# Kernel optimization log

Measured on AMD Instinct MI355X. Metric: run time of the kernel, lower is better.

The kernel has to match this reference:

```python
import jax, jax.numpy as jnp
import numpy as np

N, E, F_IN, EDIM, H = 50000, 1600000, 128, 16, 4
C1, C2, G, NCLS = 32, 8, 64, 10
NEG_SLOPE = 0.2


def setup_inputs() -> dict:
    key = jax.random.key(0)
    ks = jax.random.split(key, 20)
    s = 0.1
    inp = {
        "x": jax.random.normal(ks[0], (N, F_IN), jnp.float32),
        "edge_index": jax.random.randint(ks[1], (2, E), 0, N, dtype=jnp.int32),
        "edge_attr": jax.random.normal(ks[2], (E, EDIM), jnp.float32),
        "batch": jnp.sort(jax.random.randint(ks[3], (N,), 0, G, dtype=jnp.int32)),
        # layer 1 params (PyG GATConv: shared lin for src/dst, no lin bias)
        "W1": jax.random.normal(ks[4], (F_IN, H * C1), jnp.float32) * s,
        "as1": jax.random.normal(ks[5], (H, C1), jnp.float32) * s,
        "ad1": jax.random.normal(ks[6], (H, C1), jnp.float32) * s,
        "We1": jax.random.normal(ks[7], (EDIM, H * C1), jnp.float32) * s,
        "ae1": jax.random.normal(ks[8], (H, C1), jnp.float32) * s,
        "b1": jnp.zeros((H * C1,), jnp.float32),
        # layer 2 params
        "W2": jax.random.normal(ks[9], (H * C1, H * C2), jnp.float32) * s,
        "as2": jax.random.normal(ks[10], (H, C2), jnp.float32) * s,
        "ad2": jax.random.normal(ks[11], (H, C2), jnp.float32) * s,
        "We2": jax.random.normal(ks[12], (EDIM, H * C2), jnp.float32) * s,
        "ae2": jax.random.normal(ks[13], (H, C2), jnp.float32) * s,
        "b2": jnp.zeros((H * C2,), jnp.float32),
        # final linear
        "Wfc": jax.random.normal(ks[14], (H * C2, NCLS), jnp.float32) * s,
        "bfc": jnp.zeros((NCLS,), jnp.float32),
    }
    return inp


def _add_self_loops(src, dst, edge_attr):
    # PyG default: add_self_loops=True, fill_value='mean' (mean of incoming edge attrs)
    deg = jax.ops.segment_sum(jnp.ones((E,), jnp.float32), dst, num_segments=N)
    loop_attr = jax.ops.segment_sum(edge_attr, dst, num_segments=N) / jnp.maximum(deg, 1.0)[:, None]
    loop = jnp.arange(N, dtype=src.dtype)
    return (jnp.concatenate([src, loop]), jnp.concatenate([dst, loop]),
            jnp.concatenate([edge_attr, loop_attr], axis=0))


def _gat_layer(x, src, dst, ea, W, a_src, a_dst, We, a_e, b, heads, ch):
    n = x.shape[0]
    h = (x @ W).reshape(n, heads, ch)                 # [N,H,C]
    he = (ea @ We).reshape(-1, heads, ch)             # [Ef,H,C]
    al_src = jnp.einsum('nhc,hc->nh', h, a_src)       # [N,H]
    al_dst = jnp.einsum('nhc,hc->nh', h, a_dst)
    al_e = jnp.einsum('ehc,hc->eh', he, a_e)          # [Ef,H]
    alpha = al_src[src] + al_dst[dst] + al_e
    alpha = jax.nn.leaky_relu(alpha, NEG_SLOPE)
    # edge softmax grouped by destination node
    amax = jax.ops.segment_max(alpha, dst, num_segments=n)
    alpha = jnp.exp(alpha - amax[dst])
    denom = jax.ops.segment_sum(alpha, dst, num_segments=n)
    alpha = alpha / (denom[dst] + 1e-16)
    out = jax.ops.segment_sum(h[src] * alpha[..., None], dst, num_segments=n)  # [N,H,C]
    return out.reshape(n, heads * ch) + b


def reference(x, edge_index, edge_attr, batch, W1, as1, ad1, We1, ae1, b1,
              W2, as2, ad2, We2, ae2, b2, Wfc, bfc):
    src, dst = edge_index[0], edge_index[1]
    src, dst, ea = _add_self_loops(src, dst, edge_attr)
    h = jax.nn.relu(_gat_layer(x, src, dst, ea, W1, as1, ad1, We1, ae1, b1, H, C1))
    h = jax.nn.relu(_gat_layer(h, src, dst, ea, W2, as2, ad2, We2, ae2, b2, H, C2))
    # global mean pool over graphs
    cnt = jax.ops.segment_sum(jnp.ones((N,), jnp.float32), batch, num_segments=G)
    pooled = jax.ops.segment_sum(h, batch, num_segments=G) / jnp.maximum(cnt, 1.0)[:, None]
    return pooled @ Wfc + bfc
```

## Files before the change

### kernel.cpp

```cpp
#include <hip/hip_runtime.h>
#include <hip/hip_fp16.h>
#include <math.h>

typedef float4 f4;
#define NEG_SLOPE 0.2f
#define NBMAX 1024
#define BIN_CHUNK 8192

union h4pack { float2 f; __half2 h[2]; };

__global__ void k_prep(const float* __restrict__ We1, const float* __restrict__ ae1,
                       const float* __restrict__ We2, const float* __restrict__ ae2,
                       float* __restrict__ M) {
    int t = threadIdx.x;
    if (t >= 128) return;
    int sel = t >> 6, i = t & 63, d = i >> 2, h = i & 3;
    const float* W  = sel ? We2 : We1;
    const float* ae = sel ? ae2 : ae1;
    int C = sel ? 8 : 32, ncol = sel ? 32 : 128;
    float s = 0.f;
    for (int c = 0; c < C; ++c) s += W[d * ncol + h * C + c] * ae[h * C + c];
    M[sel * 64 + d * 4 + h] = s;
}

__global__ __launch_bounds__(256) void k_bhist(const int* __restrict__ ei,
                                               int* __restrict__ bcnt, int E, int NB) {
    __shared__ int hist[NBMAX];
    for (int i = threadIdx.x; i < NB; i += 256) hist[i] = 0;
    __syncthreads();
    int stride = gridDim.x * 256;
    for (int e = blockIdx.x * 256 + threadIdx.x; e < E; e += stride)
        atomicAdd(&hist[ei[E + e] >> 6], 1);
    __syncthreads();
    for (int i = threadIdx.x; i < NB; i += 256) {
        int h = hist[i];
        if (h) atomicAdd(&bcnt[i], h);
    }
}

__global__ void k_bscan(const int* __restrict__ bcnt, int* __restrict__ bprefix,
                        int* __restrict__ bcursor, int NB) {
    __shared__ int ts[NBMAX];
    int t = threadIdx.x;
    ts[t] = (t < NB) ? bcnt[t] : 0;
    __syncthreads();
    for (int off = 1; off < 1024; off <<= 1) {
        int v = (t >= off) ? ts[t - off] : 0;
        __syncthreads();
        ts[t] += v;
        __syncthreads();
    }
    int excl = (t == 0) ? 0 : ts[t - 1];
    if (t <= NB) {
        bprefix[t] = excl;
        if (t < NB) bcursor[t] = excl;
    }
}

__global__ void k_ale_lin(const float* __restrict__ ea, const float* __restrict__ Mbuf,
                          __half* __restrict__ ale1_e, __half* __restrict__ ale2_e, int E) {
    __shared__ float Ms[128];
    if (threadIdx.x < 128) Ms[threadIdx.x] = Mbuf[threadIdx.x];
    __syncthreads();
    int e = blockIdx.x * 256 + threadIdx.x;
    if (e >= E) return;
    const f4* row = (const f4*)(ea + (size_t)e * 16);
    f4 r0 = row[0], r1 = row[1], r2 = row[2], r3 = row[3];
    float a[16] = { r0.x, r0.y, r0.z, r0.w, r1.x, r1.y, r1.z, r1.w,
                    r2.x, r2.y, r2.z, r2.w, r3.x, r3.y, r3.z, r3.w };
    float s10 = 0.f, s11 = 0.f, s12 = 0.f, s13 = 0.f;
    float s20 = 0.f, s21 = 0.f, s22 = 0.f, s23 = 0.f;
#pragma unroll
    for (int dd = 0; dd < 16; ++dd) {
        float av = a[dd];
        s10 += av * Ms[dd * 4 + 0]; s11 += av * Ms[dd * 4 + 1];
        s12 += av * Ms[dd * 4 + 2]; s13 += av * Ms[dd * 4 + 3];
        s20 += av * Ms[64 + dd * 4 + 0]; s21 += av * Ms[64 + dd * 4 + 1];
        s22 += av * Ms[64 + dd * 4 + 2]; s23 += av * Ms[64 + dd * 4 + 3];
    }
    h4pack p1, p2;
    p1.h[0] = __floats2half2_rn(s10, s11); p1.h[1] = __floats2half2_rn(s12, s13);
    p2.h[0] = __floats2half2_rn(s20, s21); p2.h[1] = __floats2half2_rn(s22, s23);
    ((float2*)ale1_e)[e] = p1.f;
    ((float2*)ale2_e)[e] = p2.f;
}

__global__ __launch_bounds__(256) void k_bin(const int* __restrict__ ei,
                                             int* __restrict__ bcursor,
                                             int2* __restrict__ binned, int E, int NB) {
    __shared__ int hist[NBMAX], base[NBMAX], cur[NBMAX];
    for (int i = threadIdx.x; i < NB; i += 256) { hist[i] = 0; cur[i] = 0; }
    __syncthreads();
    int e0 = blockIdx.x * BIN_CHUNK;
    int e1 = min(e0 + BIN_CHUNK, E);
    for (int e = e0 + threadIdx.x; e < e1; e += 256)
        atomicAdd(&hist[ei[E + e] >> 6], 1);
    __syncthreads();
    for (int i = threadIdx.x; i < NB; i += 256) {
        int h = hist[i];
        if (h) base[i] = atomicAdd(&bcursor[i], h);
    }
    __syncthreads();
    for (int e = e0 + threadIdx.x; e < e1; e += 256) {
        int sr = ei[e], d = ei[E + e];
        int b = d >> 6;
        int loc = base[b] + atomicAdd(&cur[b], 1);
        binned[loc] = make_int2(sr, ((d & 63) << 26) | e);
    }
}

__global__ __launch_bounds__(256) void k_csr(const int2* __restrict__ binned,
                                             const int* __restrict__ bprefix,
                                             int* __restrict__ offsets,
                                             int2* __restrict__ csr_se,
                                             int N, int E, int NB) {
    __shared__ int nhist[64], noff[65];
    int b = blockIdx.x;
    if (threadIdx.x < 64) nhist[threadIdx.x] = 0;
    __syncthreads();
    int lo = bprefix[b], hi = bprefix[b + 1];
    for (int s = lo + threadIdx.x; s < hi; s += 256)
        atomicAdd(&nhist[(binned[s].y >> 26) & 63], 1);
    __syncthreads();
    if (threadIdx.x == 0) {
        int run = 0;
        for (int i = 0; i < 64; ++i) { noff[i] = run; run += nhist[i]; }
        noff[64] = run;
    }
    __syncthreads();
    int nlo = b << 6;
    int nbn = min(64, N - nlo);
    if (threadIdx.x < nbn) offsets[nlo + threadIdx.x] = lo + noff[threadIdx.x];
    if (b == NB - 1 && threadIdx.x == 0) offsets[N] = E;
    if (threadIdx.x < 64) nhist[threadIdx.x] = 0;
    __syncthreads();
    for (int s = lo + threadIdx.x; s < hi; s += 256) {
        int2 r = binned[s];
        int dl = (r.y >> 26) & 63;
        int slot = lo + noff[dl] + atomicAdd(&nhist[dl], 1);
        csr_se[slot] = make_int2(r.x, r.y & 0x03FFFFFF);
    }
}

template<int NOUT, int ROWS>
__global__ __launch_bounds__(256) void k_gemm(const float* __restrict__ X,
                                              const float* __restrict__ W,
                                              __half* __restrict__ Hout, int N) {
    __shared__ __align__(16) float xs[ROWS][128];
    int row0 = blockIdx.x * ROWS;
    int tid = threadIdx.x;
    constexpr int NF4 = ROWS * 32;
    const f4* x4 = (const f4*)X;
    for (int i = tid; i < NF4; i += 256) {
        int r = i >> 5, k4 = i & 31;
        f4 v;
        if (row0 + r < N) v = x4[(size_t)(row0 + r) * 32 + k4];
        else { v.x = v.y = v.z = v.w = 0.f; }
        ((f4*)&xs[r][0])[k4] = v;
    }
    __syncthreads();
    constexpr int GRP = 256 / NOUT;
    constexpr int PR  = ROWS / GRP;
    int col = tid % NOUT, rg = tid / NOUT;
    float acc[PR];
#pragma unroll
    for (int r = 0; r < PR; ++r) acc[r] = 0.f;
    for (int k = 0; k < 128; ++k) {
        float w = W[k * NOUT + col];
#pragma unroll
        for (int r = 0; r < PR; ++r) acc[r] += xs[rg + r * GRP][k] * w;
    }
#pragma unroll
    for (int r = 0; r < PR; ++r) {
        int row = row0 + rg + r * GRP;
        if (row < N) Hout[(size_t)row * NOUT + col] = __float2half(acc[r]);
    }
}

template<int C>
__global__ void k_al(const __half* __restrict__ Hm, const float* __restrict__ as_,
                     const float* __restrict__ ad_, float* __restrict__ als,
                     float* __restrict__ ald, int N) {
    int idx = blockIdx.x * 256 + threadIdx.x;
    int n = idx >> 2, h = idx & 3;
    if (n >= N) return;
    constexpr int CH = C / 4;
    const __half2* h2p = (const __half2*)(Hm + (size_t)n * C + h * CH);
    float a = 0.f, b = 0.f;
#pragma unroll
    for (int c = 0; c < CH / 2; ++c) {
        float2 v = __half22float2(h2p[c]);
        a += v.x * as_[h * CH + 2 * c] + v.y * as_[h * CH + 2 * c + 1];
        b += v.x * ad_[h * CH + 2 * c] + v.y * ad_[h * CH + 2 * c + 1];
    }
    als[n * 4 + h] = a;
    ald[n * 4 + h] = b;
}

__global__ __launch_bounds__(256) void k_alpha_node(const __half* __restrict__ ale_e,
                                                    __half* __restrict__ alpha_csr,
                                                    const int2* __restrict__ csr_se,
                                                    const float* __restrict__ als,
                                                    const float* __restrict__ ald,
                                                    const int* __restrict__ offsets,
                                                    float* __restrict__ rden,
                                                    float* __restrict__ selfa, int N) {
    int n = (blockIdx.x * 256 + threadIdx.x) >> 6;
    int lane = threadIdx.x & 63;
    if (n >= N) return;
    int j = lane >> 2, h = lane & 3;
    int s0 = offsets[n], s1 = offsets[n + 1];
    float aldn = ald[n * 4 + h];
    float den = 0.f, asum = 0.f;
    for (int base = s0; base < s1; base += 16) {
        int s = base + j;
        if (s < s1) {
            int2 se = csr_se[s];
            float ale = __half2float(ale_e[(size_t)se.y * 4 + h]);
            float v = als[se.x * 4 + h] + aldn + ale;
            v = (v > 0.f) ? v : NEG_SLOPE * v;
            float e = __expf(v);
            alpha_csr[s * 4 + h] = __float2half(e);
            den += e; asum += ale;
        }
    }
    den  += __shfl_xor(den, 4);  den  += __shfl_xor(den, 8);
    den  += __shfl_xor(den, 16); den  += __shfl_xor(den, 32);
    asum += __shfl_xor(asum, 4);  asum += __shfl_xor(asum, 8);
    asum += __shfl_xor(asum, 16); asum += __shfl_xor(asum, 32);
    if (j == 0) {
        float rdeg = 1.f / fmaxf((float)(s1 - s0), 1.f);
        float v = als[n * 4 + h] + aldn + asum * rdeg;
        v = (v > 0.f) ? v : NEG_SLOPE * v;
        float es = __expf(v);
        selfa[n * 4 + h] = es;
        rden[n * 4 + h] = 1.f / (den + es + 1e-16f);
    }
}

__global__ __launch_bounds__(256) void k_agg1s(const __half* __restrict__ h16,
                                               const __half* __restrict__ alpha16,
                                               const float* __restrict__ rden,
                                               const float* __restrict__ selfa,
                                               const int* __restrict__ offsets,
                                               const int2* __restrict__ csr_se,
                                               const float* __restrict__ bias,
                                               float* __restrict__ Out, int N) {
    int xcd  = blockIdx.x & 7;
    int hd   = xcd & 3;
    int half = xcd >> 2;
    int nblk = (blockIdx.x >> 3) * 2 + half;
    int n = nblk * 4 + (threadIdx.x >> 6);
    if (n >= N) return;
    int lane = threadIdx.x & 63;
    int j = lane >> 4;
    int p = lane & 15;
    int s0 = offsets[n], s1 = offsets[n + 1];
    const __half2* H2 = (const __half2*)h16;
    float acc0 = 0.f, acc1 = 0.f;
    int e1 = s1 - 1;
    for (int s = s0 + j; s < s1; s += 8) {
        int sA = s;
        int sB = min(s + 4, e1);
        int srcA = csr_se[sA].x, srcB = csr_se[sB].x;
        float aA = __half2float(alpha16[(size_t)sA * 4 + hd]);
        float aB = (s + 4 <= e1) ? __half2float(alpha16[(size_t)sB * 4 + hd]) : 0.f;
        __half2 hA = H2[(size_t)srcA * 64 + hd * 16 + p];
        __half2 hB = H2[(size_t)srcB * 64 + hd * 16 + p];
        float2 fA = __half22float2(hA), fB = __half22float2(hB);
        acc0 = fmaf(aA, fA.x, acc0); acc1 = fmaf(aA, fA.y, acc1);
        acc0 = fmaf(aB, fB.x, acc0); acc1 = fmaf(aB, fB.y, acc1);
    }
    acc0 += __shfl_xor(acc0, 16); acc0 += __shfl_xor(acc0, 32);
    acc1 += __shfl_xor(acc1, 16); acc1 += __shfl_xor(acc1, 32);
    if (j == 0) {
        float sa = selfa[n * 4 + hd];
        float2 hn = __half22float2(H2[(size_t)n * 64 + hd * 16 + p]);
        acc0 = fmaf(sa, hn.x, acc0);
        acc1 = fmaf(sa, hn.y, acc1);
        float rd = rden[n * 4 + hd];
        float2 bv = ((const float2*)bias)[hd * 16 + p];
        float2 o;
        o.x = fmaxf(fmaf(acc0, rd, bv.x), 0.f);
        o.y = fmaxf(fmaf(acc1, rd, bv.y), 0.f);
        ((float2*)Out)[(size_t)n * 64 + hd * 16 + p] = o;
    }
}

__global__ __launch_bounds__(256) void k_aggf32(const __half* __restrict__ h16,
                                                const __half* __restrict__ alpha16,
                                                const float* __restrict__ rden,
                                                const float* __restrict__ selfa,
                                                const int* __restrict__ offsets,
                                                const int2* __restrict__ csr_se,
                                                const float* __restrict__ bias,
                                                float* __restrict__ Out, int N) {
    int n = (blockIdx.x * 256 + threadIdx.x) >> 6;
    int lane = threadIdx.x & 63;
    if (n >= N) return;
    int j = lane >> 4;
    int p = lane & 15;
    int hd = p >> 2;
    int s0 = offsets[n], s1 = offsets[n + 1];
    const __half2* H2 = (const __half2*)h16;
    float acc0 = 0.f, acc1 = 0.f;
    int e1 = s1 - 1;
    for (int s = s0 + j; s < s1; s += 8) {
        int sA = s;
        int sB = min(s + 4, e1);
        int srcA = csr_se[sA].x, srcB = csr_se[sB].x;
        float aA = __half2float(alpha16[(size_t)sA * 4 + hd]);
        float aB = (s + 4 <= e1) ? __half2float(alpha16[(size_t)sB * 4 + hd]) : 0.f;
        __half2 hA = H2[(size_t)srcA * 16 + p];
        __half2 hB = H2[(size_t)srcB * 16 + p];
        float2 fA = __half22float2(hA), fB = __half22float2(hB);
        acc0 = fmaf(aA, fA.x, acc0); acc1 = fmaf(aA, fA.y, acc1);
        acc0 = fmaf(aB, fB.x, acc0); acc1 = fmaf(aB, fB.y, acc1);
    }
    acc0 += __shfl_xor(acc0, 16); acc0 += __shfl_xor(acc0, 32);
    acc1 += __shfl_xor(acc1, 16); acc1 += __shfl_xor(acc1, 32);
    if (j == 0) {
        float sa = selfa[n * 4 + hd];
        float2 hn = __half22float2(H2[(size_t)n * 16 + p]);
        acc0 = fmaf(sa, hn.x, acc0);
        acc1 = fmaf(sa, hn.y, acc1);
        float rd = rden[n * 4 + hd];
        float2 bv = ((const float2*)bias)[p];
        float2 o;
        o.x = fmaxf(fmaf(acc0, rd, bv.x), 0.f);
        o.y = fmaxf(fmaf(acc1, rd, bv.y), 0.f);
        ((float2*)Out)[(size_t)n * 16 + p] = o;
    }
}

__global__ void k_gbound(const int* __restrict__ batch, int* __restrict__ gstart, int N, int G) {
    int g = threadIdx.x;
    if (g > G) return;
    int lo = 0, hi = N;
    while (lo < hi) {
        int mid = (lo + hi) >> 1;
        if (batch[mid] < g) lo = mid + 1; else hi = mid;
    }
    gstart[g] = lo;
}

__global__ __launch_bounds__(256) void k_pool_grp(const float* __restrict__ out2,
                                                  const int* __restrict__ gstart,
                                                  float* __restrict__ pooled, int G) {
    __shared__ float red[8][32];
    int g = blockIdx.x;
    int t = threadIdx.x, c = t & 31, r = t >> 5;
    int s0 = gstart[g], s1 = gstart[g + 1];
    float acc = 0.f;
    for (int n = s0 + r; n < s1; n += 8) acc += out2[(size_t)n * 32 + c];
    red[r][c] = acc;
    __syncthreads();
    if (r == 0) {
        float s = red[0][c];
#pragma unroll
        for (int i = 1; i < 8; ++i) s += red[i][c];
        pooled[g * 32 + c] = s;
    }
}

__global__ void k_final(const float* __restrict__ pooled, const int* __restrict__ gstart,
                        const float* __restrict__ Wfc, const float* __restrict__ bfc,
                        float* __restrict__ out) {
    int t = threadIdx.x;
    if (t >= 640) return;
    int g = t / 10, cls = t % 10;
    float rc = 1.f / fmaxf((float)(gstart[g + 1] - gstart[g]), 1.f);
    float acc = bfc[cls];
    for (int c = 0; c < 32; ++c) acc += pooled[g * 32 + c] * rc * Wfc[c * 10 + cls];
    out[g * 10 + cls] = acc;
}

extern "C" void kernel_launch(void* const* d_in, const int* in_sizes, int n_in,
                              void* d_out, int out_size, void* d_ws, size_t ws_size,
                              hipStream_t stream) {
    const float* x    = (const float*)d_in[0];
    const int*   ei   = (const int*)  d_in[1];
    const float* ea   = (const float*)d_in[2];
    const int*   batch= (const int*)  d_in[3];
    const float* W1   = (const float*)d_in[4];
    const float* as1  = (const float*)d_in[5];
    const float* ad1  = (const float*)d_in[6];
    const float* We1  = (const float*)d_in[7];
    const float* ae1  = (const float*)d_in[8];
    const float* b1   = (const float*)d_in[9];
    const float* W2   = (const float*)d_in[10];
    const float* as2  = (const float*)d_in[11];
    const float* ad2  = (const float*)d_in[12];
    const float* We2  = (const float*)d_in[13];
    const float* ae2  = (const float*)d_in[14];
    const float* b2   = (const float*)d_in[15];
    const float* Wfc  = (const float*)d_in[16];
    const float* bfc  = (const float*)d_in[17];
    float* out = (float*)d_out;

    const int N  = in_sizes[3];
    const int E  = in_sizes[1] / 2;
    const int G  = 64;
    const int NB = (N + 63) >> 6;

    char* w = (char*)d_ws;
    size_t off = 0;
    auto alloc = [&](size_t bytes) -> void* {
        void* p = w + off;
        off = (off + bytes + 255) & ~(size_t)255;
        return p;
    };
    int*    bcnt       = (int*)   alloc((size_t)NBMAX * 4);
    int*    bprefix    = (int*)   alloc((size_t)(NBMAX + 1) * 4);
    int*    bcursor    = (int*)   alloc((size_t)NBMAX * 4);
    int*    offsets    = (int*)   alloc((size_t)(N + 1) * 4);
    int2*   binned     = (int2*)  alloc((size_t)E * 8);
    __half* ale1_e     = (__half*)alloc((size_t)E * 4 * 2);
    __half* ale2_e     = (__half*)alloc((size_t)E * 4 * 2);
    int2*   csr_se     = (int2*)  alloc((size_t)E * 8);
    float*  Mbuf       = (float*) alloc(128 * 4);
    __half* h16        = (__half*)alloc((size_t)N * 128 * 2);
    float*  out1       = (float*) alloc((size_t)N * 128 * 4);
    float*  als        = (float*) alloc((size_t)N * 4 * 4);
    float*  ald        = (float*) alloc((size_t)N * 4 * 4);
    float*  rden       = (float*) alloc((size_t)N * 4 * 4);
    float*  selfa      = (float*) alloc((size_t)N * 4 * 4);
    int*    gstart     = (int*)   alloc((G + 1) * 4);
    float*  pooled     = (float*) alloc(G * 32 * 4);
    __half* alpha_csr  = (__half*)binned;
    float*  out2 = out1;

    const int eb  = (E + 255) / 256;
    const int nb4 = (N + 3) / 4;
    const int agg1_grid = 8 * (((N + 3) / 4 + 1) / 2);

    hipMemsetAsync(bcnt, 0, (size_t)NBMAX * 4, stream);

    k_prep<<<1, 128, 0, stream>>>(We1, ae1, We2, ae2, Mbuf);
    k_bhist<<<128, 256, 0, stream>>>(ei, bcnt, E, NB);
    k_bscan<<<1, 1024, 0, stream>>>(bcnt, bprefix, bcursor, NB);
    k_ale_lin<<<eb, 256, 0, stream>>>(ea, Mbuf, ale1_e, ale2_e, E);
    k_bin<<<(E + BIN_CHUNK - 1) / BIN_CHUNK, 256, 0, stream>>>(ei, bcursor, binned, E, NB);
    k_csr<<<NB, 256, 0, stream>>>(binned, bprefix, offsets, csr_se, N, E, NB);
    k_gbound<<<1, 128, 0, stream>>>(batch, gstart, N, G);

    k_gemm<128, 16><<<(N + 15) / 16, 256, 0, stream>>>(x, W1, h16, N);
    k_al<128><<<(N * 4 + 255) / 256, 256, 0, stream>>>(h16, as1, ad1, als, ald, N);
    k_alpha_node<<<nb4, 256, 0, stream>>>(ale1_e, alpha_csr, csr_se, als, ald, offsets, rden, selfa, N);
    k_agg1s<<<agg1_grid, 256, 0, stream>>>(h16, alpha_csr, rden, selfa, offsets, csr_se, b1, out1, N);

    k_gemm<32, 64><<<(N + 63) / 64, 256, 0, stream>>>(out1, W2, h16, N);
    k_al<32><<<(N * 4 + 255) / 256, 256, 0, stream>>>(h16, as2, ad2, als, ald, N);
    k_alpha_node<<<nb4, 256, 0, stream>>>(ale2_e, alpha_csr, csr_se, als, ald, offsets, rden, selfa, N);
    k_aggf32<<<nb4, 256, 0, stream>>>(h16, alpha_csr, rden, selfa, offsets, csr_se, b2, out2, N);

    k_pool_grp<<<G, 256, 0, stream>>>(out2, gstart, pooled, G);
    k_final<<<1, 640, 0, stream>>>(pooled, gstart, Wfc, bfc, out);
}
```

Measured before the change: 416.6 us.

## Use head-planar feature layout and split CSR into separate src/eid arrays

```diff
diff --git a/kernel.cpp b/kernel.cpp
--- a/kernel.cpp
+++ b/kernel.cpp
@@ -112,7 +112,8 @@
 __global__ __launch_bounds__(256) void k_csr(const int2* __restrict__ binned,
                                              const int* __restrict__ bprefix,
                                              int* __restrict__ offsets,
-                                             int2* __restrict__ csr_se,
+                                             int* __restrict__ csr_src,
+                                             int* __restrict__ csr_eid,
                                              int N, int E, int NB) {
     __shared__ int nhist[64], noff[65];
     int b = blockIdx.x;
@@ -138,11 +139,12 @@
         int2 r = binned[s];
         int dl = (r.y >> 26) & 63;
         int slot = lo + noff[dl] + atomicAdd(&nhist[dl], 1);
-        csr_se[slot] = make_int2(r.x, r.y & 0x03FFFFFF);
-    }
-}
-
-template<int NOUT, int ROWS>
+        csr_src[slot] = r.x;
+        csr_eid[slot] = r.y & 0x03FFFFFF;
+    }
+}
+
+template<int NOUT, int ROWS, bool PL>
 __global__ __launch_bounds__(256) void k_gemm(const float* __restrict__ X,
                                               const float* __restrict__ W,
                                               __half* __restrict__ Hout, int N) {
@@ -173,11 +175,16 @@
 #pragma unroll
     for (int r = 0; r < PR; ++r) {
         int row = row0 + rg + r * GRP;
-        if (row < N) Hout[(size_t)row * NOUT + col] = __float2half(acc[r]);
-    }
-}
-
-template<int C>
+        if (row < N) {
+            if constexpr (PL)
+                Hout[(size_t)(col >> 5) * N * 32 + (size_t)row * 32 + (col & 31)] = __float2half(acc[r]);
+            else
+                Hout[(size_t)row * NOUT + col] = __float2half(acc[r]);
+        }
+    }
+}
+
+template<int C, bool PL>
 __global__ void k_al(const __half* __restrict__ Hm, const float* __restrict__ as_,
                      const float* __restrict__ ad_, float* __restrict__ als,
                      float* __restrict__ ald, int N) {
@@ -185,7 +192,8 @@
     int n = idx >> 2, h = idx & 3;
     if (n >= N) return;
     constexpr int CH = C / 4;
-    const __half2* h2p = (const __half2*)(Hm + (size_t)n * C + h * CH);
+    const __half2* h2p = PL ? (const __half2*)(Hm + (size_t)h * N * 32 + (size_t)n * 32)
+                            : (const __half2*)(Hm + (size_t)n * C + h * CH);
     float a = 0.f, b = 0.f;
 #pragma unroll
     for (int c = 0; c < CH / 2; ++c) {
@@ -199,7 +207,8 @@
 
 __global__ __launch_bounds__(256) void k_alpha_node(const __half* __restrict__ ale_e,
                                                     __half* __restrict__ alpha_csr,
-                                                    const int2* __restrict__ csr_se,
+                                                    const int* __restrict__ csr_src,
+                                                    const int* __restrict__ csr_eid,
                                                     const float* __restrict__ als,
                                                     const float* __restrict__ ald,
                                                     const int* __restrict__ offsets,
@@ -215,9 +224,10 @@
     for (int base = s0; base < s1; base += 16) {
         int s = base + j;
         if (s < s1) {
-            int2 se = csr_se[s];
-            float ale = __half2float(ale_e[(size_t)se.y * 4 + h]);
-            float v = als[se.x * 4 + h] + aldn + ale;
+            int src = csr_src[s];
+            int eid = csr_eid[s];
+            float ale = __half2float(ale_e[(size_t)eid * 4 + h]);
+            float v = als[src * 4 + h] + aldn + ale;
             v = (v > 0.f) ? v : NEG_SLOPE * v;
             float e = __expf(v);
             alpha_csr[s * 4 + h] = __float2half(e);
@@ -238,35 +248,32 @@
     }
 }
 
-__global__ __launch_bounds__(256) void k_agg1s(const __half* __restrict__ h16,
-                                               const __half* __restrict__ alpha16,
-                                               const float* __restrict__ rden,
-                                               const float* __restrict__ selfa,
-                                               const int* __restrict__ offsets,
-                                               const int2* __restrict__ csr_se,
-                                               const float* __restrict__ bias,
-                                               float* __restrict__ Out, int N) {
-    int xcd  = blockIdx.x & 7;
-    int hd   = xcd & 3;
-    int half = xcd >> 2;
-    int nblk = (blockIdx.x >> 3) * 2 + half;
-    int n = nblk * 4 + (threadIdx.x >> 6);
+__global__ __launch_bounds__(256) void k_aggp(const __half* __restrict__ h16,
+                                              const __half* __restrict__ alpha16,
+                                              const float* __restrict__ rden,
+                                              const float* __restrict__ selfa,
+                                              const int* __restrict__ offsets,
+                                              const int* __restrict__ csr_src,
+                                              const float* __restrict__ bias,
+                                              float* __restrict__ Out, int N) {
+    int hd = blockIdx.y;
+    int n = (blockIdx.x * 256 + threadIdx.x) >> 6;
     if (n >= N) return;
     int lane = threadIdx.x & 63;
     int j = lane >> 4;
     int p = lane & 15;
     int s0 = offsets[n], s1 = offsets[n + 1];
-    const __half2* H2 = (const __half2*)h16;
+    const __half2* Hp = (const __half2*)(h16 + (size_t)hd * N * 32);
     float acc0 = 0.f, acc1 = 0.f;
     int e1 = s1 - 1;
     for (int s = s0 + j; s < s1; s += 8) {
         int sA = s;
         int sB = min(s + 4, e1);
-        int srcA = csr_se[sA].x, srcB = csr_se[sB].x;
+        int srcA = csr_src[sA], srcB = csr_src[sB];
         float aA = __half2float(alpha16[(size_t)sA * 4 + hd]);
         float aB = (s + 4 <= e1) ? __half2float(alpha16[(size_t)sB * 4 + hd]) : 0.f;
-        __half2 hA = H2[(size_t)srcA * 64 + hd * 16 + p];
-        __half2 hB = H2[(size_t)srcB * 64 + hd * 16 + p];
+        __half2 hA = Hp[(size_t)srcA * 16 + p];
+        __half2 hB = Hp[(size_t)srcB * 16 + p];
         float2 fA = __half22float2(hA), fB = __half22float2(hB);
         acc0 = fmaf(aA, fA.x, acc0); acc1 = fmaf(aA, fA.y, acc1);
         acc0 = fmaf(aB, fB.x, acc0); acc1 = fmaf(aB, fB.y, acc1);
@@ -275,7 +282,7 @@
     acc1 += __shfl_xor(acc1, 16); acc1 += __shfl_xor(acc1, 32);
     if (j == 0) {
         float sa = selfa[n * 4 + hd];
-        float2 hn = __half22float2(H2[(size_t)n * 64 + hd * 16 + p]);
+        float2 hn = __half22float2(Hp[(size_t)n * 16 + p]);
         acc0 = fmaf(sa, hn.x, acc0);
         acc1 = fmaf(sa, hn.y, acc1);
         float rd = rden[n * 4 + hd];
@@ -292,7 +299,7 @@
                                                 const float* __restrict__ rden,
                                                 const float* __restrict__ selfa,
                                                 const int* __restrict__ offsets,
-                                                const int2* __restrict__ csr_se,
+                                                const int* __restrict__ csr_src,
                                                 const float* __restrict__ bias,
                                                 float* __restrict__ Out, int N) {
     int n = (blockIdx.x * 256 + threadIdx.x) >> 6;
@@ -308,7 +315,7 @@
     for (int s = s0 + j; s < s1; s += 8) {
         int sA = s;
         int sB = min(s + 4, e1);
-        int srcA = csr_se[sA].x, srcB = csr_se[sB].x;
+        int srcA = csr_src[sA], srcB = csr_src[sB];
         float aA = __half2float(alpha16[(size_t)sA * 4 + hd]);
         float aB = (s + 4 <= e1) ? __half2float(alpha16[(size_t)sB * 4 + hd]) : 0.f;
         __half2 hA = H2[(size_t)srcA * 16 + p];
@@ -417,7 +424,8 @@
     int2*   binned     = (int2*)  alloc((size_t)E * 8);
     __half* ale1_e     = (__half*)alloc((size_t)E * 4 * 2);
     __half* ale2_e     = (__half*)alloc((size_t)E * 4 * 2);
-    int2*   csr_se     = (int2*)  alloc((size_t)E * 8);
+    int*    csr_src    = (int*)   alloc((size_t)E * 4);
+    int*    csr_eid    = (int*)   alloc((size_t)E * 4);
     float*  Mbuf       = (float*) alloc(128 * 4);
     __half* h16        = (__half*)alloc((size_t)N * 128 * 2);
     float*  out1       = (float*) alloc((size_t)N * 128 * 4);
@@ -432,7 +440,6 @@
 
     const int eb  = (E + 255) / 256;
     const int nb4 = (N + 3) / 4;
-    const int agg1_grid = 8 * (((N + 3) / 4 + 1) / 2);
 
     hipMemsetAsync(bcnt, 0, (size_t)NBMAX * 4, stream);
 
@@ -441,18 +448,18 @@
     k_bscan<<<1, 1024, 0, stream>>>(bcnt, bprefix, bcursor, NB);
     k_ale_lin<<<eb, 256, 0, stream>>>(ea, Mbuf, ale1_e, ale2_e, E);
     k_bin<<<(E + BIN_CHUNK - 1) / BIN_CHUNK, 256, 0, stream>>>(ei, bcursor, binned, E, NB);
-    k_csr<<<NB, 256, 0, stream>>>(binned, bprefix, offsets, csr_se, N, E, NB);
+    k_csr<<<NB, 256, 0, stream>>>(binned, bprefix, offsets, csr_src, csr_eid, N, E, NB);
     k_gbound<<<1, 128, 0, stream>>>(batch, gstart, N, G);
 
-    k_gemm<128, 16><<<(N + 15) / 16, 256, 0, stream>>>(x, W1, h16, N);
-    k_al<128><<<(N * 4 + 255) / 256, 256, 0, stream>>>(h16, as1, ad1, als, ald, N);
-    k_alpha_node<<<nb4, 256, 0, stream>>>(ale1_e, alpha_csr, csr_se, als, ald, offsets, rden, selfa, N);
-    k_agg1s<<<agg1_grid, 256, 0, stream>>>(h16, alpha_csr, rden, selfa, offsets, csr_se, b1, out1, N);
-
-    k_gemm<32, 64><<<(N + 63) / 64, 256, 0, stream>>>(out1, W2, h16, N);
-    k_al<32><<<(N * 4 + 255) / 256, 256, 0, stream>>>(h16, as2, ad2, als, ald, N);
-    k_alpha_node<<<nb4, 256, 0, stream>>>(ale2_e, alpha_csr, csr_se, als, ald, offsets, rden, selfa, N);
-    k_aggf32<<<nb4, 256, 0, stream>>>(h16, alpha_csr, rden, selfa, offsets, csr_se, b2, out2, N);
+    k_gemm<128, 16, true><<<(N + 15) / 16, 256, 0, stream>>>(x, W1, h16, N);
+    k_al<128, true><<<(N * 4 + 255) / 256, 256, 0, stream>>>(h16, as1, ad1, als, ald, N);
+    k_alpha_node<<<nb4, 256, 0, stream>>>(ale1_e, alpha_csr, csr_src, csr_eid, als, ald, offsets, rden, selfa, N);
+    k_aggp<<<dim3(nb4, 4), 256, 0, stream>>>(h16, alpha_csr, rden, selfa, offsets, csr_src, b1, out1, N);
+
+    k_gemm<32, 64, false><<<(N + 63) / 64, 256, 0, stream>>>(out1, W2, h16, N);
+    k_al<32, false><<<(N * 4 + 255) / 256, 256, 0, stream>>>(h16, as2, ad2, als, ald, N);
+    k_alpha_node<<<nb4, 256, 0, stream>>>(ale2_e, alpha_csr, csr_src, csr_eid, als, ald, offsets, rden, selfa, N);
+    k_aggf32<<<nb4, 256, 0, stream>>>(h16, alpha_csr, rden, selfa, offsets, csr_src, b2, out2, N);
 
     k_pool_grp<<<G, 256, 0, stream>>>(out2, gstart, pooled, G);
     k_final<<<1, 640, 0, stream>>>(pooled, gstart, Wfc, bfc, out);
```

New measurement: 411.5 us. Within noise of the previous version (-1.2%).
